# Kernel optimization log

Measured on AMD Instinct MI355X. Metric: run time of the kernel, lower is better.

Reference implementation:

```python
import jax, jax.numpy as jnp
from jax import lax
import numpy as np

B = 2; C = 128; H = 128; W = 128; NPIX = H * W
HTH = 184; HTW = 180; NBINS = HTH * HTW
NSPH = 16384; KHT = 8; KSPH = 16
N0, N1, N2 = 1024, 256, 64
K0, K1, K2 = 8, 8, 8
EPS = 1e-5


def setup_inputs() -> dict:
    key = jax.random.key(0)
    ks = jax.random.split(key, 24)
    f32 = jnp.float32
    inp = {}
    inp["image"] = jax.random.normal(ks[0], (B, C, H, W), f32)
    inp["bn_gamma"] = jnp.ones((C,), f32)
    inp["bn_beta"] = jnp.zeros((C,), f32)
    inp["ht_idx"] = jax.random.randint(ks[1], (NBINS, KHT), 0, NPIX, jnp.int32)
    inp["ht_w"] = jax.random.uniform(ks[2], (NBINS, KHT), f32)
    inp["w_htconv"] = jax.random.normal(ks[3], (3, 3, C, C), f32) / np.sqrt(9.0 * C)
    inp["htbn_gamma"] = jnp.ones((C,), f32)
    inp["htbn_beta"] = jnp.zeros((C,), f32)
    inp["sph_idx"] = jax.random.randint(ks[4], (NSPH, KSPH), 0, NBINS, jnp.int32)
    inp["sph_w"] = jax.random.uniform(ks[5], (NSPH, KSPH), f32)
    inp["w_sc"] = jax.random.normal(ks[6], (3, 64, C), f32) / np.sqrt(1.0 * C)
    inp["b_sc"] = jnp.zeros((3, 64), f32)
    inp["scbn_gamma"] = jnp.ones((3, 64), f32)
    inp["scbn_beta"] = jnp.zeros((3, 64), f32)
    inp["dgcn_w"] = jax.random.normal(ks[7], (3, 4, 128, 64), f32) / np.sqrt(128.0)
    inp["dgcn_b"] = jnp.zeros((3, 4, 64), f32)
    inp["dgcn_hw"] = jax.random.normal(ks[8], (3, 64), f32) / 8.0
    inp["dgcn_hb"] = jnp.zeros((3,), f32)
    inp["ind0"] = jax.random.randint(ks[9], (B, N0), 0, NSPH, jnp.int32)
    inp["ind1"] = jax.random.randint(ks[10], (B, 3, N1), 0, NSPH, jnp.int32)
    inp["ind2"] = jax.random.randint(ks[11], (B, 3, N2), 0, NSPH, jnp.int32)
    # kNN-style edges: structured centers (each node repeated k times), random neighbors
    c0 = jnp.tile(jnp.repeat(jnp.arange(N0, dtype=jnp.int32), K0)[None], (B, 1))
    inp["edge0"] = jnp.stack([c0, jax.random.randint(ks[12], (B, N0 * K0), 0, N0, jnp.int32)], 1)
    c1 = jnp.broadcast_to(jnp.repeat(jnp.arange(N1, dtype=jnp.int32), K1)[None, None], (B, 3, N1 * K1))
    inp["edge1"] = jnp.stack([c1, jax.random.randint(ks[13], (B, 3, N1 * K1), 0, N1, jnp.int32)], 2)
    c2 = jnp.broadcast_to(jnp.repeat(jnp.arange(N2, dtype=jnp.int32), K2)[None, None], (B, 3, N2 * K2))
    inp["edge2"] = jnp.stack([c2, jax.random.randint(ks[14], (B, 3, N2 * K2), 0, N2, jnp.int32)], 2)
    inp["target0"] = jax.random.randint(ks[15], (B, N0), 0, 2, jnp.int32)
    inp["target1"] = jax.random.randint(ks[16], (B * 3, N1), 0, 2, jnp.int32)
    inp["target2"] = jax.random.randint(ks[17], (B * 3, N2), 0, 2, jnp.int32)
    return inp


def _bn2d(x, g, b):
    m = x.mean((0, 2, 3), keepdims=True)
    v = x.var((0, 2, 3), keepdims=True)
    return g[None, :, None, None] * (x - m) * lax.rsqrt(v + EPS) + b[None, :, None, None]


def _sphere(x_htf, sph_idx, sph_w, ind):
    # x_htf: [B,C,NBINS]; ind: [B,S] -> weighted gather of HT bins per sphere node
    mi = sph_idx[ind]          # [B,S,K]
    mw = sph_w[ind]            # [B,S,K]
    g = jax.vmap(lambda xb, ib: xb[:, ib])(x_htf, mi)   # [B,C,S,K]
    return (g * mw[:, None]).sum(-1)                    # [B,C,S]


def _sconv(x, w, b, g, be):
    # 1x1 conv [B,C,S]->[B,64,S] + BN1d (batch stats) + ReLU
    y = jnp.einsum('oc,bcs->bos', w, x) + b[None, :, None]
    m = y.mean((0, 2), keepdims=True)
    v = y.var((0, 2), keepdims=True)
    return jax.nn.relu(g[None, :, None] * (y - m) * lax.rsqrt(v + EPS) + be[None, :, None])


def _dgcn(x, edge, ws, bs, hw, hb, n, k):
    # x: [Bg,n,64]; edge: [Bg,2,n*k] (row0=center, row1=neighbor); 4 EdgeConv layers
    for i in range(4):
        xc = jnp.take_along_axis(x, edge[:, 0, :, None], axis=1)   # [Bg,n*k,Cin]
        xn = jnp.take_along_axis(x, edge[:, 1, :, None], axis=1)
        h = jax.nn.relu(jnp.concatenate([xc, xn - xc], -1) @ ws[i] + bs[i])
        x = h.reshape(x.shape[0], n, k, -1).max(2)                 # max over neighbors
    return x @ hw + hb                                             # [Bg,n] logits


def _bce(logits, target):
    t = target.astype(logits.dtype)
    l = jnp.maximum(logits, 0.0) - logits * t + jnp.log1p(jnp.exp(-jnp.abs(logits)))
    pos = t > 0.5
    npos = jnp.maximum(pos.sum(), 1).astype(l.dtype)
    nneg = jnp.maximum((~pos).sum(), 1).astype(l.dtype)
    return jnp.where(pos, l, 0.0).sum() / npos, jnp.where(pos, 0.0, l).sum() / nneg


def _forward(image, bn_gamma, bn_beta, ht_idx, ht_w, w_htconv, htbn_gamma, htbn_beta,
             sph_idx, sph_w, w_sc, b_sc, scbn_gamma, scbn_beta,
             dgcn_w, dgcn_b, dgcn_hw, dgcn_hb,
             ind0, ind1, ind2, edge0, edge1, edge2, target0, target1, target2):
    x = jax.nn.relu(_bn2d(image, bn_gamma, bn_beta))
    xf = x.reshape(B, C, NPIX)
    # Hough voting: each HT bin accumulates KHT weighted pixels
    ht = (xf[:, :, ht_idx] * ht_w).sum(-1).reshape(B, C, HTH, HTW)
    hc = lax.conv_general_dilated(ht, w_htconv, (1, 1), 'SAME',
                                  dimension_numbers=('NCHW', 'HWIO', 'NCHW'))
    x_htf = jax.nn.relu(_bn2d(hc, htbn_gamma, htbn_beta)).reshape(B, C, NBINS)

    # scale 0
    x0 = _sconv(_sphere(x_htf, sph_idx, sph_w, ind0),
                w_sc[0], b_sc[0], scbn_gamma[0], scbn_beta[0]).transpose(0, 2, 1)
    x0 = _dgcn(x0, edge0, dgcn_w[0], dgcn_b[0], dgcn_hw[0], dgcn_hb[0], N0, K0)   # [B,N0]
    # scale 1 (3 vanishing-point branches folded into batch)
    x1 = _sconv(_sphere(x_htf, sph_idx, sph_w, ind1.reshape(B, -1)),
                w_sc[1], b_sc[1], scbn_gamma[1], scbn_beta[1]).transpose(0, 2, 1)
    x1 = _dgcn(x1.reshape(B * 3, N1, 64), edge1.reshape(B * 3, 2, N1 * K1),
               dgcn_w[1], dgcn_b[1], dgcn_hw[1], dgcn_hb[1], N1, K1)              # [B*3,N1]
    # scale 2
    x2 = _sconv(_sphere(x_htf, sph_idx, sph_w, ind2.reshape(B, -1)),
                w_sc[2], b_sc[2], scbn_gamma[2], scbn_beta[2]).transpose(0, 2, 1)
    x2 = _dgcn(x2.reshape(B * 3, N2, 64), edge2.reshape(B * 3, 2, N2 * K2),
               dgcn_w[2], dgcn_b[2], dgcn_hw[2], dgcn_hb[2], N2, K2)              # [B*3,N2]

    lp0, ln0 = _bce(x0, target0)
    lp1, ln1 = _bce(x1, target1)
    lp2, ln2 = _bce(x2, target2)
    losses = jnp.stack([lp0, ln0, lp1, ln1, lp2, ln2])
    preds = jnp.concatenate([jax.nn.sigmoid(x0).reshape(B, -1),
                             jax.nn.sigmoid(x1).reshape(B, -1),
                             jax.nn.sigmoid(x2).reshape(B, -1)], axis=1)
    return losses, preds


def reference(image, bn_gamma, bn_beta, ht_idx, ht_w, w_htconv, htbn_gamma, htbn_beta,
              sph_idx, sph_w, w_sc, b_sc, scbn_gamma, scbn_beta,
              dgcn_w, dgcn_b, dgcn_hw, dgcn_hb,
              ind0, ind1, ind2, edge0, edge1, edge2, target0, target1, target2):
    return _forward(image, bn_gamma, bn_beta, ht_idx, ht_w, w_htconv, htbn_gamma, htbn_beta,
                    sph_idx, sph_w, w_sc, b_sc, scbn_gamma, scbn_beta,
                    dgcn_w, dgcn_b, dgcn_hw, dgcn_hb,
                    ind0, ind1, ind2, edge0, edge1, edge2, target0, target1, target2)
```

## Files before the change

### kernel.cpp

```cpp
#include <hip/hip_runtime.h>
#include <math.h>

#define B_ 2
#define C_ 128
#define NPIX_ 16384
#define HTH_ 184
#define HTW_ 180
#define NBINS_ 33120
#define PH_ 186
#define PW_ 184
#define NPB_ 1984
#define TOTN_ 3968
#define EPS_ 1e-5f

#define ST_HC_SUM 0
#define ST_HC_SQ  128
#define ST_SC_SUM 256
#define ST_SC_SQ  448
#define ST_LOSS   640
#define ST_IMG_S1 1472
#define ST_IMG_S2 1600

typedef __attribute__((ext_vector_type(8))) short v8s;
typedef __attribute__((ext_vector_type(4))) float v4f;

__device__ inline unsigned short f2b(float f) {
  unsigned u = __builtin_bit_cast(unsigned, f);
  unsigned r = u + 0x7fffu + ((u >> 16) & 1u);
  return (unsigned short)(r >> 16);
}
__device__ inline float b2f(unsigned short u) {
  unsigned v = ((unsigned)u) << 16;
  return __builtin_bit_cast(float, v);
}

__global__ void kprep0(const float* __restrict__ w, const float* __restrict__ dw,
                       const float* __restrict__ wsc,
                       unsigned short* __restrict__ wtb, unsigned short* __restrict__ dwb,
                       unsigned short* __restrict__ swb,
                       unsigned* __restrict__ htb2, const float* __restrict__ img,
                       float* __restrict__ st) {
  int bid = blockIdx.x;
  int tid = threadIdx.x;
  if (bid < 1612) {
    int idx = bid*256 + tid;
    if (idx < 147456) {
      int tap = idx >> 14, z = idx & 16383;
      int j = z & 7, lane = (z >> 3) & 63, nt = (z >> 9) & 7, kt = (z >> 12) & 3;
      int l = lane & 15, q = lane >> 4;
      int co = nt*16 + l, ci = kt*32 + q*8 + j;
      wtb[idx] = f2b(w[(tap*C_ + ci)*C_ + co]);
    } else if (idx < 245760) {
      int i2 = idx - 147456;
      int sl = i2 >> 13, z = i2 & 8191;
      int j = z & 7, lane = (z >> 3) & 63, nt = (z >> 9) & 3, kt = (z >> 11) & 3;
      int l = lane & 15, q = lane >> 4;
      int co = nt*16 + l, cc = kt*32 + q*8 + j;
      dwb[i2] = f2b(dw[(sl*128 + cc)*64 + co]);
    } else if (idx < 270336) {
      int i3 = idx - 245760;
      int s = i3 >> 13, z = i3 & 8191;
      int j = z & 7, lane = (z >> 3) & 63, nt = (z >> 9) & 3, kt = (z >> 11) & 3;
      int l = lane & 15, q = lane >> 4;
      int co = nt*16 + l, cc = kt*32 + q*8 + j;
      swb[i3] = f2b(wsc[(s*64 + co)*128 + cc]);
    } else if (idx < 412672) {
      int i = idx - 270336;
      int d = i & 63;
      int cell = i >> 6;
      int b = cell / 1112, j = cell % 1112;
      int y, x;
      if (j < 184) { y = 0; x = j; }
      else if (j < 368) { y = 185; x = j - 184; }
      else { int c = j - 368; int xi = c / 186; y = c % 186; x = xi == 0 ? 0 : 180 + xi; }
      htb2[((size_t)(b*PH_ + y)*PW_ + x)*64 + d] = 0u;
    }
  } else {
    int kb = bid - 1612;
    int c = kb >> 3, chunk = kb & 7;
    float s1 = 0.f, s2 = 0.f;
    for (int i = chunk*4096 + tid; i < (chunk+1)*4096; i += 256) {
      int b = i >> 14, p = i & (NPIX_-1);
      float v = img[((size_t)(b*C_ + c))*NPIX_ + p];
      s1 += v; s2 += v*v;
    }
    __shared__ float r1[256], r2[256];
    r1[tid] = s1; r2[tid] = s2; __syncthreads();
    for (int off = 128; off; off >>= 1) {
      if (tid < off) { r1[tid] += r1[tid+off]; r2[tid] += r2[tid+off]; }
      __syncthreads();
    }
    if (tid == 0) {
      atomicAdd(&st[ST_IMG_S1 + c], r1[0]);
      atomicAdd(&st[ST_IMG_S2 + c], r2[0]);
    }
  }
}

__global__ void k2_bnrelu_t(const float* __restrict__ img, const float* __restrict__ st,
                            const float* __restrict__ g, const float* __restrict__ be,
                            unsigned short* __restrict__ xt) {
  __shared__ float tile[32*65];
  __shared__ float ash[32], dsh[32];
  int p0 = blockIdx.x*64, c0 = blockIdx.y*32, b = blockIdx.z;
  int tid = threadIdx.x;
  if (tid < 32) {
    int c = c0 + tid;
    float n = (float)(B_*NPIX_);
    float m = st[ST_IMG_S1+c]/n;
    float var = st[ST_IMG_S2+c]/n - m*m;
    float a = g[c]*rsqrtf(var + EPS_);
    ash[tid] = a; dsh[tid] = be[c] - a*m;
  }
  __syncthreads();
  for (int r = 0; r < 8; r++) {
    int flat = tid + r*256;
    int row = flat >> 6, col = flat & 63;
    float v = img[((size_t)(b*C_ + c0 + row))*NPIX_ + p0 + col];
    tile[row*65 + col] = fmaxf(ash[row]*v + dsh[row], 0.f);
  }
  __syncthreads();
  for (int r = 0; r < 4; r++) {
    int flat = (tid + r*256)*2;
    int pl = flat >> 5, cl = flat & 31;
    unsigned lo = f2b(tile[cl*65 + pl]);
    unsigned hi = f2b(tile[(cl+1)*65 + pl]);
    *(unsigned*)&xt[((size_t)b*NPIX_ + p0 + pl)*C_ + c0 + cl] = lo | (hi << 16);
  }
}

__global__ void k3_hough(const unsigned* __restrict__ xt2, const int* __restrict__ hidx,
                         const float* __restrict__ hwt, unsigned* __restrict__ htb2) {
  int tid = threadIdx.x;
  int wv = __builtin_amdgcn_readfirstlane(tid >> 6);
  int bin = blockIdx.x*4 + wv;
  int b = blockIdx.y;
  int lane = tid & 63;
  const unsigned* base = xt2 + (size_t)b*NPIX_*64 + lane;
  float acc0 = 0.f, acc1 = 0.f;
  #pragma unroll
  for (int k = 0; k < 8; k++) {
    int p = hidx[bin*8 + k];
    float w = hwt[bin*8 + k];
    unsigned dv = base[(size_t)p*64];
    acc0 += w * b2f((unsigned short)(dv & 0xffff));
    acc1 += w * b2f((unsigned short)(dv >> 16));
  }
  int y = bin / HTW_, x = bin - y*HTW_;
  unsigned lo = f2b(acc0), hi = f2b(acc1);
  htb2[((size_t)(b*PH_ + y + 1)*PW_ + (x+1))*64 + lane] = lo | (hi << 16);
}

__global__ __launch_bounds__(256) void k4_mfma(
    const unsigned short* __restrict__ htb, const unsigned short* __restrict__ wtb,
    unsigned short* __restrict__ hcb, float* __restrict__ st) {
  __shared__ char smem[65536];
  int tid = threadIdx.x;
  int wav = tid >> 6, lane = tid & 63;
  int quad = lane >> 4, l16 = lane & 15;
  int b = blockIdx.y;
  int p0 = blockIdx.x*128 + wav*32;
  size_t ab[2];
  #pragma unroll
  for (int t = 0; t < 2; t++) {
    int px = p0 + t*16 + l16; if (px > NBINS_-1) px = NBINS_-1;
    int y = px / HTW_, x = px % HTW_;
    ab[t] = (((size_t)(b*PH_ + y))*PW_ + x)*C_ + quad*8;
  }
  v4f acc[2][8];
  #pragma unroll
  for (int t = 0; t < 2; t++)
    #pragma unroll
    for (int nt = 0; nt < 8; nt++) acc[t][nt] = (v4f){0,0,0,0};

  {
    const uint4* src = (const uint4*)wtb;
    uint4* dst = (uint4*)smem;
    #pragma unroll
    for (int s = 0; s < 8; s++) dst[tid + s*256] = src[tid + s*256];
  }
  __syncthreads();
  for (int tap = 0; tap < 9; tap++) {
    uint4 wreg[8];
    if (tap < 8) {
      const uint4* src = (const uint4*)(wtb + (tap+1)*16384);
      #pragma unroll
      for (int s = 0; s < 8; s++) wreg[s] = src[tid + s*256];
    }
    const char* cur = smem + (tap & 1)*32768;
    int dy = tap/3, dx = tap - dy*3;
    int toff = (dy*PW_ + dx)*C_;
    v8s a[2][4];
    #pragma unroll
    for (int t = 0; t < 2; t++)
      #pragma unroll
      for (int kt = 0; kt < 4; kt++)
        a[t][kt] = *(const v8s*)&htb[ab[t] + toff + kt*32];
    #pragma unroll
    for (int kt = 0; kt < 4; kt++) {
      #pragma unroll
      for (int nt = 0; nt < 8; nt++) {
        v8s bf = *(const v8s*)(cur + ((((kt*8 + nt)*64) + lane) << 4));
        acc[0][nt] = __builtin_amdgcn_mfma_f32_16x16x32_bf16(a[0][kt], bf, acc[0][nt], 0, 0, 0);
        acc[1][nt] = __builtin_amdgcn_mfma_f32_16x16x32_bf16(a[1][kt], bf, acc[1][nt], 0, 0, 0);
      }
    }
    if (tap < 8) {
      uint4* dst = (uint4*)(smem + ((tap+1) & 1)*32768);
      #pragma unroll
      for (int s = 0; s < 8; s++) dst[tid + s*256] = wreg[s];
    }
    __syncthreads();
  }
  float* red = (float*)smem;
  float s1[8], s2[8];
  #pragma unroll
  for (int nt = 0; nt < 8; nt++) { s1[nt] = 0.f; s2[nt] = 0.f; }
  #pragma unroll
  for (int t = 0; t < 2; t++) {
    int pbase = p0 + t*16 + quad*4;
    #pragma unroll
    for (int nt = 0; nt < 8; nt++) {
      int co = nt*16 + l16;
      #pragma unroll
      for (int reg = 0; reg < 4; reg++) {
        int po = pbase + reg;
        if (po < NBINS_) {
          float v = acc[t][nt][reg];
          hcb[((size_t)b*NBINS_ + po)*C_ + co] = f2b(v);
          s1[nt] += v; s2[nt] += v*v;
        }
      }
    }
  }
  int slot = wav*4 + quad;
  #pragma unroll
  for (int nt = 0; nt < 8; nt++) red[(nt*16 + l16)*17 + slot] = s1[nt];
  __syncthreads();
  if (tid < 128) {
    float s = 0.f;
    #pragma unroll
    for (int k = 0; k < 16; k++) s += red[tid*17 + k];
    atomicAdd(&st[ST_HC_SUM + tid], s);
  }
  __syncthreads();
  #pragma unroll
  for (int nt = 0; nt < 8; nt++) red[(nt*16 + l16)*17 + slot] = s2[nt];
  __syncthreads();
  if (tid < 128) {
    float s = 0.f;
    #pragma unroll
    for (int k = 0; k < 16; k++) s += red[tid*17 + k];
    atomicAdd(&st[ST_HC_SQ + tid], s);
  }
}

__global__ __launch_bounds__(256) void k67_sphconv(
    const unsigned* __restrict__ hcb2, const float* __restrict__ g, const float* __restrict__ be,
    const int* __restrict__ sph_idx, const float* __restrict__ sph_w,
    const int* __restrict__ ind0, const int* __restrict__ ind1, const int* __restrict__ ind2,
    const unsigned short* __restrict__ swb, const float* __restrict__ b_sc,
    float* __restrict__ y, float* __restrict__ st) {
  __shared__ unsigned short E[16*136];
  int tid = threadIdx.x;
  int gn0 = blockIdx.x*8;
  int nb0 = gn0 % NPB_;
  int s = nb0 < 1024 ? 0 : (nb0 < 1792 ? 1 : 2);
  int wv = tid >> 6, lane = tid & 63;
  int quad = lane >> 4, l16 = lane & 15;
  {
    int c0 = lane*2, c1 = c0 + 1;
    float n = (float)(B_*NBINS_);
    float m0 = st[ST_HC_SUM + c0]/n, m1 = st[ST_HC_SUM + c1]/n;
    float va0 = st[ST_HC_SQ + c0]/n - m0*m0, va1 = st[ST_HC_SQ + c1]/n - m1*m1;
    float a0 = g[c0]*rsqrtf(va0 + EPS_), a1 = g[c1]*rsqrtf(va1 + EPS_);
    float d0 = be[c0] - a0*m0, d1 = be[c1] - a1*m1;
    #pragma unroll
    for (int i = 0; i < 2; i++) {
      int node_l = wv*2 + i;
      int gn = gn0 + node_l;
      int b = gn / NPB_, nb = gn % NPB_;
      int v;
      if (nb < 1024) v = ind0[b*1024 + nb];
      else if (nb < 1792) v = ind1[b*768 + nb - 1024];
      else v = ind2[b*192 + nb - 1792];
      v = __builtin_amdgcn_readfirstlane(v);
      const unsigned* base = hcb2 + (size_t)b*NBINS_*64 + lane;
      float acc0 = 0.f, acc1 = 0.f;
      #pragma unroll
      for (int k = 0; k < 16; k++) {
        int mi = sph_idx[v*16 + k];
        float mw = sph_w[v*16 + k];
        unsigned dv = base[(size_t)mi*64];
        acc0 += mw * fmaxf(a0*b2f((unsigned short)(dv & 0xffff)) + d0, 0.f);
        acc1 += mw * fmaxf(a1*b2f((unsigned short)(dv >> 16)) + d1, 0.f);
      }
      unsigned lo = f2b(acc0), hi = f2b(acc1);
      *(unsigned*)&E[node_l*136 + c0] = lo | (hi << 16);
    }
  }
  __syncthreads();
  v4f acc = (v4f){0,0,0,0};
  const unsigned short* wb = swb + s*8192 + wv*512;
  #pragma unroll
  for (int kt = 0; kt < 4; kt++) {
    v8s a = *(const v8s*)&E[l16*136 + quad*8 + kt*32];
    v8s bf = *(const v8s*)&wb[kt*2048 + lane*8];
    acc = __builtin_amdgcn_mfma_f32_16x16x32_bf16(a, bf, acc, 0, 0, 0);
  }
  float bias = b_sc[s*64 + wv*16 + l16];
  float s1 = 0.f, s2 = 0.f;
  #pragma unroll
  for (int reg = 0; reg < 4; reg++) {
    int row = quad*4 + reg;
    if (quad < 2) {
      float val = acc[reg] + bias;
      y[(size_t)(gn0 + row)*64 + wv*16 + l16] = val;
      s1 += val; s2 += val*val;
    }
  }
  s1 += __shfl_xor(s1, 16);
  s2 += __shfl_xor(s2, 16);
  if (quad == 0) {
    atomicAdd(&st[ST_SC_SUM + s*64 + wv*16 + l16], s1);
    atomicAdd(&st[ST_SC_SQ  + s*64 + wv*16 + l16], s2);
  }
}

__global__ __launch_bounds__(256) void k10_dgcn(
    const void* __restrict__ xin_, unsigned short* __restrict__ xout,
    const int* __restrict__ edge0, const int* __restrict__ edge1, const int* __restrict__ edge2,
    const unsigned short* __restrict__ dwb, const float* __restrict__ db,
    const float* __restrict__ st, const float* __restrict__ scg, const float* __restrict__ scb,
    int layer, int usebn) {
  __shared__ unsigned short E[64*136];
  __shared__ float ash[64], dsh[64];
  int tid = threadIdx.x;
  int bid = blockIdx.x;
  int s, node_base, le_blk, span; const int* ec;
  if (bid < 256) {
    s = 0; int b = bid >> 7; node_base = b*NPB_; le_blk = (bid & 127)*64;
    span = 8192; ec = edge0 + b*2*8192;
  } else if (bid < 448) {
    int j = bid - 256; s = 1; int seg = j >> 5; int b = seg/3, vp = seg%3;
    node_base = b*NPB_ + 1024 + vp*256; le_blk = (j & 31)*64;
    span = 2048; ec = edge1 + ((b*3+vp)*2)*2048;
  } else {
    int j = bid - 448; s = 2; int seg = j >> 3; int b = seg/3, vp = seg%3;
    node_base = b*NPB_ + 1792 + vp*64; le_blk = (j & 7)*64;
    span = 512; ec = edge2 + ((b*3+vp)*2)*512;
  }
  const int* en = ec + span;
  if (usebn) {
    if (tid < 64) {
      float n = s==0 ? 2048.f : (s==1 ? 1536.f : 384.f);
      float m = st[ST_SC_SUM + s*64 + tid]/n;
      float var = st[ST_SC_SQ + s*64 + tid]/n - m*m;
      float a = scg[s*64 + tid]*rsqrtf(var + EPS_);
      ash[tid] = a; dsh[tid] = scb[s*64 + tid] - a*m;
    }
    __syncthreads();
  }
  {
    int e_l = tid >> 2, part = tid & 3;
    int h = part >> 1, cb = (part & 1)*32;
    int e = le_blk + e_l;
    int ci = ec[e], ni = en[e];
    if (usebn) {
      const float* xc = (const float*)xin_ + (size_t)(node_base + ci)*64 + cb;
      const float* xn = (const float*)xin_ + (size_t)(node_base + ni)*64 + cb;
      float4 xc4[8], xn4[8];
      #pragma unroll
      for (int q = 0; q < 8; q++) xc4[q] = *(const float4*)&xc[q*4];
      if (h) {
        #pragma unroll
        for (int q = 0; q < 8; q++) xn4[q] = *(const float4*)&xn[q*4];
      }
      #pragma unroll
      for (int c8 = 0; c8 < 32; c8 += 8) {
        v8s pk;
        #pragma unroll
        for (int j = 0; j < 8; j++) {
          int cl = c8 + j;
          int c = cb + cl;
          float xcv = ((const float*)xc4)[cl];
          float vc = fmaxf(ash[c]*xcv + dsh[c], 0.f);
          float val = vc;
          if (h) {
            float xnv = ((const float*)xn4)[cl];
            val = fmaxf(ash[c]*xnv + dsh[c], 0.f) - vc;
          }
          pk[j] = (short)f2b(val);
        }
        *(v8s*)&E[e_l*136 + h*64 + cb + c8] = pk;
      }
    } else {
      const unsigned short* xc = (const unsigned short*)xin_ + (size_t)(node_base + ci)*64 + cb;
      const unsigned short* xn = (const unsigned short*)xin_ + (size_t)(node_base + ni)*64 + cb;
      #pragma unroll
      for (int c8 = 0; c8 < 32; c8 += 8) {
        v8s vc8 = *(const v8s*)&xc[c8];
        v8s pk = vc8;
        if (h) {
          v8s vn8 = *(const v8s*)&xn[c8];
          #pragma unroll
          for (int j = 0; j < 8; j++)
            pk[j] = (short)f2b(b2f((unsigned short)vn8[j]) - b2f((unsigned short)vc8[j]));
        }
        *(v8s*)&E[e_l*136 + h*64 + cb + c8] = pk;
      }
    }
  }
  __syncthreads();
  int wave = tid >> 6, lane = tid & 63;
  int quad = lane >> 4, l16 = lane & 15;
  const unsigned short* wb = dwb + (size_t)(s*4 + layer)*8192;
  v4f acc[4];
  #pragma unroll
  for (int nt = 0; nt < 4; nt++) acc[nt] = (v4f){0,0,0,0};
  #pragma unroll
  for (int kt = 0; kt < 4; kt++) {
    v8s a = *(const v8s*)&E[(wave*16 + l16)*136 + quad*8 + kt*32];
    #pragma unroll
    for (int nt = 0; nt < 4; nt++) {
      v8s bf = *(const v8s*)&wb[((kt*4 + nt)*64 + lane)*8];
      acc[nt] = __builtin_amdgcn_mfma_f32_16x16x32_bf16(a, bf, acc[nt], 0, 0, 0);
    }
  }
  #pragma unroll
  for (int nt = 0; nt < 4; nt++) {
    float bias = db[(s*4 + layer)*64 + nt*16 + l16];
    float m = fmaxf(fmaxf(acc[nt][0], acc[nt][1]), fmaxf(acc[nt][2], acc[nt][3]));
    m = fmaxf(m + bias, 0.f);
    float other = __shfl_xor(m, 16);
    m = fmaxf(m, other);
    if ((quad & 1) == 0) {
      int node_l = wave*2 + (quad >> 1);
      xout[(size_t)(node_base + (le_blk >> 3) + node_l)*64 + nt*16 + l16] = f2b(m);
    }
  }
}

__global__ __launch_bounds__(256) void k11_head(
    const unsigned short* __restrict__ x, const float* __restrict__ hw, const float* __restrict__ hb,
    const int* __restrict__ t0, const int* __restrict__ t1, const int* __restrict__ t2,
    float* __restrict__ out, float* __restrict__ st) {
  __shared__ float shw[192];
  int tid = threadIdx.x;
  if (tid < 192) shw[tid] = hw[tid];
  __syncthreads();
  int gn = blockIdx.x*256 + tid;
  bool valid = gn < TOTN_;
  int g = valid ? gn : TOTN_-1;
  int b = g / NPB_, nb = g % NPB_;
  int s, tg;
  if (nb < 1024) { s = 0; tg = t0[b*1024 + nb]; }
  else if (nb < 1792) { s = 1; int j = nb-1024; tg = t1[(b*3 + (j>>8))*256 + (j&255)]; }
  else { s = 2; int j = nb-1792; tg = t2[(b*3 + (j>>6))*64 + (j&63)]; }
  const unsigned short* row = x + (size_t)g*64;
  float logit = hb[s];
  #pragma unroll
  for (int c8 = 0; c8 < 64; c8 += 8) {
    v8s v = *(const v8s*)&row[c8];
    #pragma unroll
    for (int j = 0; j < 8; j++)
      logit += b2f((unsigned short)v[j]) * shw[s*64 + c8 + j];
  }
  if (valid) out[6 + gn] = 1.f / (1.f + expf(-logit));
  float tf = (float)tg;
  float l = fmaxf(logit, 0.f) - logit*tf + log1pf(expf(-fabsf(logit)));
  float sp = (valid && tg) ? l : 0.f;
  float sn = (valid && !tg) ? l : 0.f;
  float cp = (valid && tg) ? 1.f : 0.f;
  float cn = (valid && !tg) ? 1.f : 0.f;
  for (int off = 32; off; off >>= 1) {
    sp += __shfl_down(sp, off);
    sn += __shfl_down(sn, off);
    cp += __shfl_down(cp, off);
    cn += __shfl_down(cn, off);
  }
  if ((tid & 63) == 0) {
    atomicAdd(&st[ST_LOSS + s*4 + 0], sp);
    atomicAdd(&st[ST_LOSS + s*4 + 1], sn);
    atomicAdd(&st[ST_LOSS + s*4 + 2], cp);
    atomicAdd(&st[ST_LOSS + s*4 + 3], cn);
  }
}

__global__ void k12_fin(const float* __restrict__ st, float* __restrict__ out) {
  int i = threadIdx.x;
  if (i < 6) {
    int s = i >> 1; int pos = !(i & 1);
    float sum = st[ST_LOSS + s*4 + (pos ? 0 : 1)];
    float cnt = st[ST_LOSS + s*4 + (pos ? 2 : 3)];
    out[i] = sum / fmaxf(cnt, 1.f);
  }
}

extern "C" void kernel_launch(void* const* d_in, const int* in_sizes, int n_in,
                              void* d_out, int out_size, void* d_ws, size_t ws_size,
                              hipStream_t stream) {
  const float* image  = (const float*)d_in[0];
  const float* bn_g   = (const float*)d_in[1];
  const float* bn_b   = (const float*)d_in[2];
  const int*   ht_idx = (const int*)  d_in[3];
  const float* ht_w   = (const float*)d_in[4];
  const float* w_conv = (const float*)d_in[5];
  const float* htbn_g = (const float*)d_in[6];
  const float* htbn_b = (const float*)d_in[7];
  const int*   sph_idx= (const int*)  d_in[8];
  const float* sph_w  = (const float*)d_in[9];
  const float* w_sc   = (const float*)d_in[10];
  const float* b_sc   = (const float*)d_in[11];
  const float* scbn_g = (const float*)d_in[12];
  const float* scbn_b = (const float*)d_in[13];
  const float* dgcn_w = (const float*)d_in[14];
  const float* dgcn_b = (const float*)d_in[15];
  const float* dgcn_hw= (const float*)d_in[16];
  const float* dgcn_hb= (const float*)d_in[17];
  const int*   ind0   = (const int*)  d_in[18];
  const int*   ind1   = (const int*)  d_in[19];
  const int*   ind2   = (const int*)  d_in[20];
  const int*   edge0  = (const int*)  d_in[21];
  const int*   edge1  = (const int*)  d_in[22];
  const int*   edge2  = (const int*)  d_in[23];
  const int*   t0     = (const int*)  d_in[24];
  const int*   t1     = (const int*)  d_in[25];
  const int*   t2     = (const int*)  d_in[26];
  float* out = (float*)d_out;

  char* ws = (char*)d_ws;
  unsigned short* x_t   = (unsigned short*)(ws);
  unsigned short* htb   = (unsigned short*)(ws +  8388608);
  unsigned short* hcb   = (unsigned short*)(ws + 25911296);
  unsigned short* wtb   = (unsigned short*)(ws + 42868736);
  unsigned short* dwb   = (unsigned short*)(ws + 43163648);
  unsigned short* swb   = (unsigned short*)(ws + 43360256);
  float*          y_sc  = (float*)(ws + 43409408);
  unsigned short* xdgA  = (unsigned short*)(ws + 44425216);
  unsigned short* xdgB  = (unsigned short*)(ws + 44933120);
  float*          st    = (float*)(ws + 45441024);

  hipMemsetAsync(st, 0, 1728*sizeof(float), stream);
  kprep0<<<2636, 256, 0, stream>>>(w_conv, dgcn_w, w_sc, wtb, dwb, swb, (unsigned*)htb, image, st);
  k2_bnrelu_t<<<dim3(256,4,2), 256, 0, stream>>>(image, st, bn_g, bn_b, x_t);
  k3_hough<<<dim3(NBINS_/4, B_), 256, 0, stream>>>((const unsigned*)x_t, ht_idx, ht_w, (unsigned*)htb);
  k4_mfma<<<dim3(259, 2), 256, 0, stream>>>(htb, wtb, hcb, st);
  k67_sphconv<<<TOTN_/8, 256, 0, stream>>>((const unsigned*)hcb, htbn_g, htbn_b, sph_idx, sph_w,
                                           ind0, ind1, ind2, swb, b_sc, y_sc, st);
  k10_dgcn<<<496, 256, 0, stream>>>((const void*)y_sc, xdgA, edge0, edge1, edge2, dwb, dgcn_b, st, scbn_g, scbn_b, 0, 1);
  k10_dgcn<<<496, 256, 0, stream>>>((const void*)xdgA, xdgB, edge0, edge1, edge2, dwb, dgcn_b, st, scbn_g, scbn_b, 1, 0);
  k10_dgcn<<<496, 256, 0, stream>>>((const void*)xdgB, xdgA, edge0, edge1, edge2, dwb, dgcn_b, st, scbn_g, scbn_b, 2, 0);
  k10_dgcn<<<496, 256, 0, stream>>>((const void*)xdgA, xdgB, edge0, edge1, edge2, dwb, dgcn_b, st, scbn_g, scbn_b, 3, 0);
  k11_head<<<16, 256, 0, stream>>>(xdgB, dgcn_hw, dgcn_hb, t0, t1, t2, out, st);
  k12_fin<<<1, 64, 0, stream>>>(st, out);
}
```

Before: 241.7 us.

## Split conv MFMA output channels across grid and fold loss finalize into head

The 3x3 MFMA conv kernel now splits its 128 output channels into two halves along a new grid dimension. Each block holds half the weights in LDS (32KB instead of 64KB) and half the accumulators, which should allow more resident blocks and twice the grid size. The cost is that the A-operand activation loads are read twice. Separately, the final loss-normalization kernel is removed: the head kernel uses a float-atomic ticket so the last block computes the six outputs, saving one launch at the cost of fence and atomic overhead.

```diff
diff --git a/kernel.cpp b/kernel.cpp
--- a/kernel.cpp
+++ b/kernel.cpp
@@ -18,6 +18,7 @@
 #define ST_SC_SUM 256
 #define ST_SC_SQ  448
 #define ST_LOSS   640
+#define ST_TICKET 652
 #define ST_IMG_S1 1472
 #define ST_IMG_S2 1600
 
@@ -151,14 +152,14 @@
   htb2[((size_t)(b*PH_ + y + 1)*PW_ + (x+1))*64 + lane] = lo | (hi << 16);
 }
 
-__global__ __launch_bounds__(256) void k4_mfma(
+__global__ __launch_bounds__(256, 4) void k4_mfma(
     const unsigned short* __restrict__ htb, const unsigned short* __restrict__ wtb,
     unsigned short* __restrict__ hcb, float* __restrict__ st) {
-  __shared__ char smem[65536];
+  __shared__ char smem[32768];
   int tid = threadIdx.x;
   int wav = tid >> 6, lane = tid & 63;
   int quad = lane >> 4, l16 = lane & 15;
-  int b = blockIdx.y;
+  int b = blockIdx.y, ch = blockIdx.z;
   int p0 = blockIdx.x*128 + wav*32;
   size_t ab[2];
   #pragma unroll
@@ -167,27 +168,37 @@
     int y = px / HTW_, x = px % HTW_;
     ab[t] = (((size_t)(b*PH_ + y))*PW_ + x)*C_ + quad*8;
   }
-  v4f acc[2][8];
+  int c0s = tid, c1s = tid + 256, c2s = tid + 512, c3s = tid + 768;
+  size_t so[4];
+  {
+    int cc[4] = {c0s, c1s, c2s, c3s};
+    #pragma unroll
+    for (int s = 0; s < 4; s++) {
+      int c = cc[s];
+      int kt = c >> 8, ntl = (c >> 6) & 3, ls = c & 63;
+      so[s] = ((size_t)((kt*8 + ch*4 + ntl)*64 + ls))*8;
+    }
+  }
+  v4f acc[2][4];
   #pragma unroll
   for (int t = 0; t < 2; t++)
     #pragma unroll
-    for (int nt = 0; nt < 8; nt++) acc[t][nt] = (v4f){0,0,0,0};
+    for (int nt = 0; nt < 4; nt++) acc[t][nt] = (v4f){0,0,0,0};
 
   {
-    const uint4* src = (const uint4*)wtb;
-    uint4* dst = (uint4*)smem;
-    #pragma unroll
-    for (int s = 0; s < 8; s++) dst[tid + s*256] = src[tid + s*256];
+    const unsigned short* src = wtb;
+    #pragma unroll
+    for (int s = 0; s < 4; s++)
+      *(uint4*)(smem + (tid + s*256)*16) = *(const uint4*)(src + so[s]);
   }
   __syncthreads();
   for (int tap = 0; tap < 9; tap++) {
-    uint4 wreg[8];
+    uint4 wreg[4];
     if (tap < 8) {
-      const uint4* src = (const uint4*)(wtb + (tap+1)*16384);
-      #pragma unroll
-      for (int s = 0; s < 8; s++) wreg[s] = src[tid + s*256];
-    }
-    const char* cur = smem + (tap & 1)*32768;
+      const unsigned short* src = wtb + (tap+1)*16384;
+      #pragma unroll
+      for (int s = 0; s < 4; s++) wreg[s] = *(const uint4*)(src + so[s]);
+    }
     int dy = tap/3, dx = tap - dy*3;
     int toff = (dy*PW_ + dx)*C_;
     v8s a[2][4];
@@ -196,32 +207,31 @@
       #pragma unroll
       for (int kt = 0; kt < 4; kt++)
         a[t][kt] = *(const v8s*)&htb[ab[t] + toff + kt*32];
+    const char* cur = smem + (tap & 1)*16384;
     #pragma unroll
     for (int kt = 0; kt < 4; kt++) {
       #pragma unroll
-      for (int nt = 0; nt < 8; nt++) {
-        v8s bf = *(const v8s*)(cur + ((((kt*8 + nt)*64) + lane) << 4));
+      for (int nt = 0; nt < 4; nt++) {
+        v8s bf = *(const v8s*)(cur + (((kt*4 + nt)*64 + lane) << 4));
         acc[0][nt] = __builtin_amdgcn_mfma_f32_16x16x32_bf16(a[0][kt], bf, acc[0][nt], 0, 0, 0);
         acc[1][nt] = __builtin_amdgcn_mfma_f32_16x16x32_bf16(a[1][kt], bf, acc[1][nt], 0, 0, 0);
       }
     }
     if (tap < 8) {
-      uint4* dst = (uint4*)(smem + ((tap+1) & 1)*32768);
-      #pragma unroll
-      for (int s = 0; s < 8; s++) dst[tid + s*256] = wreg[s];
+      char* nb = smem + ((tap+1) & 1)*16384;
+      #pragma unroll
+      for (int s = 0; s < 4; s++) *(uint4*)(nb + (tid + s*256)*16) = wreg[s];
     }
     __syncthreads();
   }
   float* red = (float*)smem;
-  float s1[8], s2[8];
-  #pragma unroll
-  for (int nt = 0; nt < 8; nt++) { s1[nt] = 0.f; s2[nt] = 0.f; }
+  float s1[4] = {0,0,0,0}, s2[4] = {0,0,0,0};
   #pragma unroll
   for (int t = 0; t < 2; t++) {
     int pbase = p0 + t*16 + quad*4;
     #pragma unroll
-    for (int nt = 0; nt < 8; nt++) {
-      int co = nt*16 + l16;
+    for (int nt = 0; nt < 4; nt++) {
+      int co = ch*64 + nt*16 + l16;
       #pragma unroll
       for (int reg = 0; reg < 4; reg++) {
         int po = pbase + reg;
@@ -235,23 +245,23 @@
   }
   int slot = wav*4 + quad;
   #pragma unroll
-  for (int nt = 0; nt < 8; nt++) red[(nt*16 + l16)*17 + slot] = s1[nt];
-  __syncthreads();
-  if (tid < 128) {
+  for (int nt = 0; nt < 4; nt++) red[(nt*16 + l16)*17 + slot] = s1[nt];
+  __syncthreads();
+  if (tid < 64) {
     float s = 0.f;
     #pragma unroll
     for (int k = 0; k < 16; k++) s += red[tid*17 + k];
-    atomicAdd(&st[ST_HC_SUM + tid], s);
-  }
-  __syncthreads();
-  #pragma unroll
-  for (int nt = 0; nt < 8; nt++) red[(nt*16 + l16)*17 + slot] = s2[nt];
-  __syncthreads();
-  if (tid < 128) {
+    atomicAdd(&st[ST_HC_SUM + ch*64 + tid], s);
+  }
+  __syncthreads();
+  #pragma unroll
+  for (int nt = 0; nt < 4; nt++) red[(nt*16 + l16)*17 + slot] = s2[nt];
+  __syncthreads();
+  if (tid < 64) {
     float s = 0.f;
     #pragma unroll
     for (int k = 0; k < 16; k++) s += red[tid*17 + k];
-    atomicAdd(&st[ST_HC_SQ + tid], s);
+    atomicAdd(&st[ST_HC_SQ + ch*64 + tid], s);
   }
 }
 
@@ -485,15 +495,20 @@
     atomicAdd(&st[ST_LOSS + s*4 + 2], cp);
     atomicAdd(&st[ST_LOSS + s*4 + 3], cn);
   }
-}
-
-__global__ void k12_fin(const float* __restrict__ st, float* __restrict__ out) {
-  int i = threadIdx.x;
-  if (i < 6) {
-    int s = i >> 1; int pos = !(i & 1);
-    float sum = st[ST_LOSS + s*4 + (pos ? 0 : 1)];
-    float cnt = st[ST_LOSS + s*4 + (pos ? 2 : 3)];
-    out[i] = sum / fmaxf(cnt, 1.f);
+  __syncthreads();
+  __threadfence();
+  if (tid == 0) {
+    unsigned t = (unsigned)atomicAdd(&st[ST_TICKET], 1.f);
+    if (t == 15.f) {}
+    if (t >= 15) {
+      #pragma unroll
+      for (int i = 0; i < 6; i++) {
+        int sc = i >> 1; int pos = !(i & 1);
+        float sum = atomicAdd(&st[ST_LOSS + sc*4 + (pos ? 0 : 1)], 0.f);
+        float cnt = atomicAdd(&st[ST_LOSS + sc*4 + (pos ? 2 : 3)], 0.f);
+        out[i] = sum / fmaxf(cnt, 1.f);
+      }
+    }
   }
 }
 
@@ -545,7 +560,7 @@
   kprep0<<<2636, 256, 0, stream>>>(w_conv, dgcn_w, w_sc, wtb, dwb, swb, (unsigned*)htb, image, st);
   k2_bnrelu_t<<<dim3(256,4,2), 256, 0, stream>>>(image, st, bn_g, bn_b, x_t);
   k3_hough<<<dim3(NBINS_/4, B_), 256, 0, stream>>>((const unsigned*)x_t, ht_idx, ht_w, (unsigned*)htb);
-  k4_mfma<<<dim3(259, 2), 256, 0, stream>>>(htb, wtb, hcb, st);
+  k4_mfma<<<dim3(259, 2, 2), 256, 0, stream>>>(htb, wtb, hcb, st);
   k67_sphconv<<<TOTN_/8, 256, 0, stream>>>((const unsigned*)hcb, htbn_g, htbn_b, sph_idx, sph_w,
                                            ind0, ind1, ind2, swb, b_sc, y_sc, st);
   k10_dgcn<<<496, 256, 0, stream>>>((const void*)y_sc, xdgA, edge0, edge1, edge2, dwb, dgcn_b, st, scbn_g, scbn_b, 0, 1);
@@ -553,5 +568,4 @@
   k10_dgcn<<<496, 256, 0, stream>>>((const void*)xdgB, xdgA, edge0, edge1, edge2, dwb, dgcn_b, st, scbn_g, scbn_b, 2, 0);
   k10_dgcn<<<496, 256, 0, stream>>>((const void*)xdgA, xdgB, edge0, edge1, edge2, dwb, dgcn_b, st, scbn_g, scbn_b, 3, 0);
   k11_head<<<16, 256, 0, stream>>>(xdgB, dgcn_hw, dgcn_hb, t0, t1, t2, out, st);
-  k12_fin<<<1, 64, 0, stream>>>(st, out);
-}
+}
```

Result: slower. 252.0 us (+4.2%).
